# Kernel tuning notes

Measured on AMD Instinct MI355X. Metric: run time of the kernel, lower is better.

## Reference

```python
import jax, jax.numpy as jnp
import numpy as np

NEG_SLOPE = 0.2  # PyG GATConv default LeakyReLU slope


def gat_layer(x, src, dst, W, a_src, a_dst, bias, num_nodes, heads, out_ch, concat):
    # x: [N, in], W: [in, heads*out_ch], a_src/a_dst: [heads, out_ch]
    h = (x @ W).reshape(num_nodes, heads, out_ch)          # [N,H,C]
    alpha_s = jnp.sum(h * a_src, axis=-1)                  # [N,H]
    alpha_d = jnp.sum(h * a_dst, axis=-1)                  # [N,H]
    e = jax.nn.leaky_relu(alpha_s[src] + alpha_d[dst], NEG_SLOPE)  # [E,H]
    # softmax over incoming edges of each destination node
    e_max = jax.ops.segment_max(e, dst, num_segments=num_nodes)   # [N,H]
    e_exp = jnp.exp(e - e_max[dst])                        # [E,H]
    denom = jax.ops.segment_sum(e_exp, dst, num_segments=num_nodes)  # [N,H]
    alpha = e_exp / denom[dst]                             # [E,H]
    msg = h[src] * alpha[:, :, None]                       # [E,H,C]
    out = jax.ops.segment_sum(msg, dst, num_segments=num_nodes)     # [N,H,C]
    if concat:
        out = out.reshape(num_nodes, heads * out_ch)
    else:
        out = out.mean(axis=1)
    return out + bias


def setup_inputs() -> dict:
    key = jax.random.key(0)
    ks = jax.random.split(key, 12)
    N, E = 50000, 800000
    IN, HID, OUT, H = 128, 32, 64, 4
    x = jax.random.normal(ks[0], (N, IN), dtype=jnp.float32)
    edge_index = jax.random.randint(ks[1], (2, E), 0, N, dtype=jnp.int32)
    s = 1.0 / np.sqrt(IN)
    W1 = jax.random.normal(ks[2], (IN, H * HID), dtype=jnp.float32) * s
    a_src1 = jax.random.normal(ks[3], (H, HID), dtype=jnp.float32) * 0.1
    a_dst1 = jax.random.normal(ks[4], (H, HID), dtype=jnp.float32) * 0.1
    b1 = jnp.zeros((H * HID,), dtype=jnp.float32)
    s2 = 1.0 / np.sqrt(H * HID)
    W2 = jax.random.normal(ks[5], (H * HID, OUT), dtype=jnp.float32) * s2
    a_src2 = jax.random.normal(ks[6], (1, OUT), dtype=jnp.float32) * 0.1
    a_dst2 = jax.random.normal(ks[7], (1, OUT), dtype=jnp.float32) * 0.1
    b2 = jnp.zeros((OUT,), dtype=jnp.float32)
    return {"x": x, "edge_index": edge_index, "W1": W1, "a_src1": a_src1,
            "a_dst1": a_dst1, "b1": b1, "W2": W2, "a_src2": a_src2,
            "a_dst2": a_dst2, "b2": b2}


def reference(x, edge_index, W1, a_src1, a_dst1, b1, W2, a_src2, a_dst2, b2):
    N = x.shape[0]
    src, dst = edge_index[0], edge_index[1]
    h = gat_layer(x, src, dst, W1, a_src1, a_dst1, b1, N, heads=4, out_ch=32, concat=True)
    h = jax.nn.elu(h)
    # dropout is identity in eval / p=0.0
    out = gat_layer(h, src, dst, W2, a_src2, a_dst2, b2, N, heads=1, out_ch=64, concat=False)
    return out
```

## Files before the change

kernel.cpp:

```cpp
#include <hip/hip_runtime.h>

#define C1 128
#define C2 64
#define CAP 96
#define NBF 2048

typedef __attribute__((ext_vector_type(8))) _Float16 half8;
typedef __attribute__((ext_vector_type(2))) _Float16 half2v;
typedef __attribute__((ext_vector_type(2))) __fp16  fp16x2;
typedef __attribute__((ext_vector_type(4))) float floatx4;

__device__ __forceinline__ float lrelu(float v) { return v > 0.f ? v : 0.2f * v; }

__device__ __forceinline__ unsigned pk2h(float a, float b) {
    union { fp16x2 p; unsigned u; } c;
    c.p = __builtin_amdgcn_cvt_pkrtz(a, b);
    return c.u;
}

__global__ __launch_bounds__(256)
void gemm1_fill_kernel(const float* __restrict__ x, const float* __restrict__ W1,
                       const float* __restrict__ asrc, const float* __restrict__ adst,
                       unsigned* __restrict__ h1d,
                       float* __restrict__ as1, float* __restrict__ ad1,
                       const int* __restrict__ ei, int* __restrict__ cursor,
                       int* __restrict__ csrc, int nbTile, int N, int E) {
    if ((int)blockIdx.x >= nbTile) {
        const int b    = blockIdx.x - nbTile;
        const int part = b & 7;
        const int bIdx = b >> 3;
        const int bpp  = NBF >> 3;
        const int lo = (int)(((long)N * part) >> 3);
        const int hi = (int)(((long)N * (part + 1)) >> 3);

        const int E4 = ((E & 3) == 0) ? (E >> 2) : 0;
        const int4* d4 = (const int4*)(ei + E);
        const int4* s4 = (const int4*)ei;
        for (int q = bIdx * 256 + threadIdx.x; q < E4; q += bpp * 256) {
            int4 dv = d4[q];
            int4 sv = s4[q];
            int dd[4] = {dv.x, dv.y, dv.z, dv.w};
            int ss[4] = {sv.x, sv.y, sv.z, sv.w};
            int pos[4];
            bool act[4];
#pragma unroll
            for (int i = 0; i < 4; ++i) {
                act[i] = (dd[i] >= lo) & (dd[i] < hi) & ((unsigned)ss[i] < (unsigned)N);
                pos[i] = act[i] ? atomicAdd(&cursor[dd[i]], 1) : 0;
            }
#pragma unroll
            for (int i = 0; i < 4; ++i)
                if (act[i] && pos[i] < CAP) csrc[dd[i] * CAP + pos[i]] = ss[i];
        }
        for (int e = E4 * 4 + bIdx * 256 + threadIdx.x; e < E; e += bpp * 256) {
            int dd = ei[E + e];
            if (dd < lo || dd >= hi) continue;
            int ss = ei[e];
            if ((unsigned)ss >= (unsigned)N) continue;
            int pp = atomicAdd(&cursor[dd], 1);
            if (pp < CAP) csrc[dd * CAP + pp] = ss;
        }
        return;
    }

    __shared__ __align__(16) unsigned short Bs[128 * 136];
    for (int i = threadIdx.x; i < 128 * 64; i += 256) {
        int col = i & 127;
        int k = (i >> 7) * 2;
        *(unsigned*)&Bs[col * 136 + k] = pk2h(W1[k * 128 + col], W1[(k + 1) * 128 + col]);
    }
    __syncthreads();

    const int lane = threadIdx.x & 63, ww = threadIdx.x >> 6;
    const int quad = lane >> 4, l16 = lane & 15;
    const int nodeBase = blockIdx.x * 64 + ww * 16;
    int arow = nodeBase + l16;
    if (arow >= N) arow = N - 1;
    const float* xp = x + (size_t)arow * C1 + quad * 8;
    half8 afr[4];
#pragma unroll
    for (int kk = 0; kk < 4; ++kk) {
        float4 a0 = *(const float4*)(xp + kk * 32);
        float4 a1 = *(const float4*)(xp + kk * 32 + 4);
        union { half8 v; unsigned u[4]; } fr;
        fr.u[0] = pk2h(a0.x, a0.y);
        fr.u[1] = pk2h(a0.z, a0.w);
        fr.u[2] = pk2h(a1.x, a1.y);
        fr.u[3] = pk2h(a1.z, a1.w);
        afr[kk] = fr.v;
    }

#pragma unroll
    for (int h = 0; h < 4; ++h) {
        floatx4 accL = {0.f, 0.f, 0.f, 0.f};
        floatx4 accH = {0.f, 0.f, 0.f, 0.f};
        const int colL = h * 32 + l16;
        const int colH = colL + 16;
        const unsigned short* bL = &Bs[colL * 136 + quad * 8];
        const unsigned short* bH = &Bs[colH * 136 + quad * 8];
#pragma unroll
        for (int kk = 0; kk < 4; ++kk) {
            half8 bfrL = *(const half8*)(bL + kk * 32);
            half8 bfrH = *(const half8*)(bH + kk * 32);
            accL = __builtin_amdgcn_mfma_f32_16x16x32_f16(afr[kk], bfrL, accL, 0, 0, 0);
            accH = __builtin_amdgcn_mfma_f32_16x16x32_f16(afr[kk], bfrH, accH, 0, 0, 0);
        }
#pragma unroll
        for (int reg = 0; reg < 4; ++reg) {
            int node = nodeBase + quad * 4 + reg;
            if (node < N) h1d[(size_t)node * 64 + h * 16 + l16] = pk2h(accL[reg], accH[reg]);
        }
        float avL = asrc[colL], dvL = adst[colL];
        float avH = asrc[colH], dvH = adst[colH];
#pragma unroll
        for (int reg = 0; reg < 4; ++reg) {
            float ts = accL[reg] * avL + accH[reg] * avH;
            float td = accL[reg] * dvL + accH[reg] * dvH;
#pragma unroll
            for (int o = 1; o < 16; o <<= 1) {
                ts += __shfl_xor(ts, o, 64);
                td += __shfl_xor(td, o, 64);
            }
            if (l16 == 0) {
                int node = nodeBase + quad * 4 + reg;
                if (node < N) {
                    as1[node * 4 + h] = ts;
                    ad1[node * 4 + h] = td;
                }
            }
        }
    }
}

__global__ __launch_bounds__(256)
void msg1_csr_kernel(const int* __restrict__ cursor, const int* __restrict__ csrc,
                     const unsigned* __restrict__ h1u, const float* __restrict__ as1,
                     const float* __restrict__ ad1, const float* __restrict__ b1,
                     unsigned* __restrict__ out1, int N) {
    __shared__ float ws[4][64];
    const int wid = threadIdx.x >> 6;
    const int d = blockIdx.x * 4 + wid;
    if (d >= N) return;
    const int lane = threadIdx.x & 63;
    const int e16 = lane & 15;
    const int head = lane >> 4;
    int dg = cursor[d]; if (dg > CAP) dg = CAP;
    const int base = d * CAP;
    const float wadh = ad1[d * 4 + head];
    float accx = 0.f, accy = 0.f, sumw = 0.f;
    for (int jj = 0; jj < dg; jj += 16) {
        int idx = jj + e16;
        if (idx >= dg) idx = dg - 1;
        const int myS = csrc[base + idx];
        unsigned rv[16];
#pragma unroll
        for (int k = 0; k < 16; ++k) {
            int s = __builtin_amdgcn_readlane(myS, k);
            rv[k] = h1u[(unsigned)s * 64u + (unsigned)lane];
        }
        float w = 0.f;
        if (jj + e16 < dg)
            w = __expf(lrelu(as1[myS * 4 + head] + wadh));
        ws[wid][lane] = w;
#pragma unroll
        for (int j = 0; j < 4; ++j) {
            float4 wf = ((const float4*)&ws[wid][head * 16])[j];
            union { unsigned u; half2v p; } c0, c1, c2, c3;
            c0.u = rv[4 * j + 0]; c1.u = rv[4 * j + 1];
            c2.u = rv[4 * j + 2]; c3.u = rv[4 * j + 3];
            sumw += (wf.x + wf.y) + (wf.z + wf.w);
            accx += wf.x * (float)c0.p[0]; accy += wf.x * (float)c0.p[1];
            accx += wf.y * (float)c1.p[0]; accy += wf.y * (float)c1.p[1];
            accx += wf.z * (float)c2.p[0]; accy += wf.z * (float)c2.p[1];
            accx += wf.w * (float)c3.p[0]; accy += wf.w * (float)c3.p[1];
        }
    }
    float inv = (sumw > 0.f) ? 1.f / sumw : 0.f;
    float rx = accx * inv + b1[32 * head + e16];
    float ry = accy * inv + b1[32 * head + e16 + 16];
    rx = rx > 0.f ? rx : expm1f(rx);
    ry = ry > 0.f ? ry : expm1f(ry);
    out1[(size_t)d * 64 + lane] = pk2h(rx, ry);
}

__global__ __launch_bounds__(256)
void gemm2_mfma_kernel(const unsigned short* __restrict__ h2, const float* __restrict__ W2,
                       const float* __restrict__ asrc, const float* __restrict__ adst,
                       unsigned* __restrict__ g2d, float* __restrict__ as2,
                       float* __restrict__ ad2, int N) {
    __shared__ __align__(16) unsigned short Bs[64 * 136];
    for (int i = threadIdx.x; i < 64 * 64; i += 256) {
        int col = i & 63;
        int p = i >> 6;
        int k0 = 32 * (p >> 4) + (p & 15);
        *(unsigned*)&Bs[col * 136 + 2 * p] = pk2h(W2[k0 * 64 + col], W2[(k0 + 16) * 64 + col]);
    }
    __syncthreads();

    const int lane = threadIdx.x & 63, ww = threadIdx.x >> 6;
    const int quad = lane >> 4, l16 = lane & 15;
    const int nodeBase = blockIdx.x * 64 + ww * 16;
    int arow = nodeBase + l16;
    if (arow >= N) arow = N - 1;
    const unsigned short* xp = h2 + (size_t)arow * C1 + quad * 8;
    half8 afr[4];
#pragma unroll
    for (int kk = 0; kk < 4; ++kk)
        afr[kk] = *(const half8*)(xp + kk * 32);

    float sacc[4] = {0.f,0.f,0.f,0.f}, dacc[4] = {0.f,0.f,0.f,0.f};
#pragma unroll
    for (int ctp = 0; ctp < 2; ++ctp) {
        floatx4 accL = {0.f, 0.f, 0.f, 0.f};
        floatx4 accH = {0.f, 0.f, 0.f, 0.f};
        const int colL = ctp * 16 + l16;
        const int colH = colL + 32;
        const unsigned short* bL = &Bs[colL * 136 + quad * 8];
        const unsigned short* bH = &Bs[colH * 136 + quad * 8];
#pragma unroll
        for (int kk = 0; kk < 4; ++kk) {
            half8 bfrL = *(const half8*)(bL + kk * 32);
            half8 bfrH = *(const half8*)(bH + kk * 32);
            accL = __builtin_amdgcn_mfma_f32_16x16x32_f16(afr[kk], bfrL, accL, 0, 0, 0);
            accH = __builtin_amdgcn_mfma_f32_16x16x32_f16(afr[kk], bfrH, accH, 0, 0, 0);
        }
#pragma unroll
        for (int reg = 0; reg < 4; ++reg) {
            int node = nodeBase + quad * 4 + reg;
            if (node < N) g2d[(size_t)node * 32 + colL] = pk2h(accL[reg], accH[reg]);
        }
        float avL = asrc[colL], dvL = adst[colL];
        float avH = asrc[colH], dvH = adst[colH];
#pragma unroll
        for (int reg = 0; reg < 4; ++reg) {
            sacc[reg] += accL[reg] * avL + accH[reg] * avH;
            dacc[reg] += accL[reg] * dvL + accH[reg] * dvH;
        }
    }
#pragma unroll
    for (int reg = 0; reg < 4; ++reg) {
        float ts = sacc[reg], td = dacc[reg];
#pragma unroll
        for (int o = 1; o < 16; o <<= 1) {
            ts += __shfl_xor(ts, o, 64);
            td += __shfl_xor(td, o, 64);
        }
        if (l16 == 0) {
            int node = nodeBase + quad * 4 + reg;
            if (node < N) { as2[node] = ts; ad2[node] = td; }
        }
    }
}

__global__ __launch_bounds__(256)
void msg2_csr_kernel(const int* __restrict__ cursor, const int* __restrict__ csrc,
                     const unsigned* __restrict__ g2u, const float* __restrict__ as2,
                     const float* __restrict__ ad2, const float* __restrict__ b2,
                     float* __restrict__ yf, int N) {
    __shared__ float wsm[4][32];
    __shared__ int   ssm[4][32];
    const int wid = threadIdx.x >> 6;
    const int d = blockIdx.x * 4 + wid;
    if (d >= N) return;
    const int lane = threadIdx.x & 63;
    const int half = lane >> 5;
    const int l32 = lane & 31;
    int dg = cursor[d]; if (dg > CAP) dg = CAP;
    const int base = d * CAP;
    const float add = ad2[d];
    float accx = 0.f, accy = 0.f, sumw = 0.f;
    for (int jj = 0; jj < dg; jj += 32) {
        int idx = jj + l32;
        if (idx >= dg) idx = dg - 1;
        const int myS = csrc[base + idx];
        float w = 0.f;
        if (jj + l32 < dg) w = __expf(lrelu(as2[myS] + add));
        ssm[wid][l32] = myS;
        wsm[wid][l32] = w;
        int4 s0 = ((const int4*)&ssm[wid][half * 16])[0];
        int4 s1 = ((const int4*)&ssm[wid][half * 16])[1];
        int4 s2 = ((const int4*)&ssm[wid][half * 16])[2];
        int4 s3 = ((const int4*)&ssm[wid][half * 16])[3];
        int ss[16] = {s0.x, s0.y, s0.z, s0.w, s1.x, s1.y, s1.z, s1.w,
                      s2.x, s2.y, s2.z, s2.w, s3.x, s3.y, s3.z, s3.w};
        unsigned rv[16];
#pragma unroll
        for (int k = 0; k < 16; ++k)
            rv[k] = g2u[(unsigned)ss[k] * 32u + (unsigned)l32];
#pragma unroll
        for (int j = 0; j < 4; ++j) {
            float4 wf = ((const float4*)&wsm[wid][half * 16])[j];
            union { unsigned u; half2v p; } c0, c1, c2, c3;
            c0.u = rv[4 * j + 0]; c1.u = rv[4 * j + 1];
            c2.u = rv[4 * j + 2]; c3.u = rv[4 * j + 3];
            sumw += (wf.x + wf.y) + (wf.z + wf.w);
            accx += wf.x * (float)c0.p[0]; accy += wf.x * (float)c0.p[1];
            accx += wf.y * (float)c1.p[0]; accy += wf.y * (float)c1.p[1];
            accx += wf.z * (float)c2.p[0]; accy += wf.z * (float)c2.p[1];
            accx += wf.w * (float)c3.p[0]; accy += wf.w * (float)c3.p[1];
        }
    }
    accx += __shfl_xor(accx, 32, 64);
    accy += __shfl_xor(accy, 32, 64);
    sumw += __shfl_xor(sumw, 32, 64);
    if (half == 0) {
        float inv = (sumw > 0.f) ? 1.f / sumw : 0.f;
        yf[(size_t)d * 64 + l32]      = accx * inv + b2[l32];
        yf[(size_t)d * 64 + 32 + l32] = accy * inv + b2[l32 + 32];
    }
}

extern "C" void kernel_launch(void* const* d_in, const int* in_sizes, int n_in,
                              void* d_out, int out_size, void* d_ws, size_t ws_size,
                              hipStream_t stream) {
    const float* x    = (const float*)d_in[0];
    const int*   ei   = (const int*)d_in[1];
    const float* W1   = (const float*)d_in[2];
    const float* a_s1 = (const float*)d_in[3];
    const float* a_d1 = (const float*)d_in[4];
    const float* b1   = (const float*)d_in[5];
    const float* W2   = (const float*)d_in[6];
    const float* a_s2 = (const float*)d_in[7];
    const float* a_d2 = (const float*)d_in[8];
    const float* b2   = (const float*)d_in[9];

    const int N = in_sizes[0] / C1;
    const int E = in_sizes[1] / 2;

    auto align16 = [](size_t v) { return (v + 15) & ~(size_t)15; };
    const size_t RF   = 16;
    const size_t RCUR = align16((size_t)N * 4);
    const size_t RSRC = align16((size_t)N * CAP * 4);
    const size_t R1   = align16((size_t)N * C1 * 4);
    const size_t R2   = align16((size_t)N * 8 * 4);

    char* base = (char*)d_ws;
    int*  cursor = (int*)(base + RF);
    int*  csrc   = (int*)(base + RF + RCUR);
    char* R1p = base + RF + RCUR + RSRC;
    char* R2p = R1p + R1;
    char* R4p = R2p + R2;
    (void)ws_size;

    unsigned* h1 = (unsigned*)R1p;
    unsigned* g2 = (unsigned*)R1p;
    float* as1 = (float*)R2p;
    float* ad1 = as1 + (size_t)N * 4;
    float* as2 = (float*)R2p;
    float* ad2 = as2 + N;
    unsigned* out1 = (unsigned*)R4p;

    const int nbTile = (N + 63) / 64;
    const int nbWave4 = (N + 3) / 4;

    hipMemsetAsync(cursor, 0, (size_t)N * 4, stream);
    gemm1_fill_kernel<<<nbTile + NBF, 256, 0, stream>>>(x, W1, a_s1, a_d1, h1,
        as1, ad1, ei, cursor, csrc, nbTile, N, E);
    msg1_csr_kernel<<<nbWave4, 256, 0, stream>>>(cursor, csrc, (const unsigned*)h1,
        as1, ad1, b1, out1, N);
    gemm2_mfma_kernel<<<nbTile, 256, 0, stream>>>((const unsigned short*)out1, W2,
        a_s2, a_d2, g2, as2, ad2, N);
    msg2_csr_kernel<<<nbWave4, 256, 0, stream>>>(cursor, csrc, (const unsigned*)g2,
        as2, ad2, b2, (float*)d_out, N);
}
```

Measured before the change: 207.0 us.

## Interleave GEMM tiles with CSR-fill blocks and shrink msg2 gather batches

The fused gemm1/fill kernel used to put all GEMM tile blocks first and the CSR fill blocks after them. It now interleaves them in groups of eight, so compute-heavy tiles and atomic-heavy fill work run on the GPU at the same time instead of one phase after the other. Separately, msg2 now processes 16 neighbours per iteration instead of 32. Each half-wave takes alternate neighbours, using a transposed weight layout in shared memory. This aims to cut wasted gather and exp work for low-degree nodes, at the cost of more loop iterations and less load-level parallelism per iteration.

```diff
diff --git a/kernel.cpp b/kernel.cpp
--- a/kernel.cpp
+++ b/kernel.cpp
@@ -24,11 +24,17 @@
                        unsigned* __restrict__ h1d,
                        float* __restrict__ as1, float* __restrict__ ad1,
                        const int* __restrict__ ei, int* __restrict__ cursor,
-                       int* __restrict__ csrc, int nbTile, int N, int E) {
-    if ((int)blockIdx.x >= nbTile) {
-        const int b    = blockIdx.x - nbTile;
-        const int part = b & 7;
-        const int bIdx = b >> 3;
+                       int* __restrict__ csrc, int nbTile, int nbg, int kg, int ze,
+                       int N, int E) {
+    const int g   = blockIdx.x >> 3;
+    const int sub = blockIdx.x & 7;
+    int tile = -1, fg = -1;
+    if (g < ze && (g % kg) == 0) tile = (g / kg) * 8 + sub;
+    else fg = (g < ze) ? (g - g / kg - 1) : (g - nbg);
+
+    if (tile < 0) {
+        const int part = sub;
+        const int bIdx = fg;
         const int bpp  = NBF >> 3;
         const int lo = (int)(((long)N * part) >> 3);
         const int hi = (int)(((long)N * (part + 1)) >> 3);
@@ -62,6 +68,7 @@
         }
         return;
     }
+    if (tile >= nbTile) return;
 
     __shared__ __align__(16) unsigned short Bs[128 * 136];
     for (int i = threadIdx.x; i < 128 * 64; i += 256) {
@@ -73,7 +80,7 @@
 
     const int lane = threadIdx.x & 63, ww = threadIdx.x >> 6;
     const int quad = lane >> 4, l16 = lane & 15;
-    const int nodeBase = blockIdx.x * 64 + ww * 16;
+    const int nodeBase = tile * 64 + ww * 16;
     int arow = nodeBase + l16;
     if (arow >= N) arow = N - 1;
     const float* xp = x + (size_t)arow * C1 + quad * 8;
@@ -257,8 +264,8 @@
                      const unsigned* __restrict__ g2u, const float* __restrict__ as2,
                      const float* __restrict__ ad2, const float* __restrict__ b2,
                      float* __restrict__ yf, int N) {
-    __shared__ float wsm[4][32];
-    __shared__ int   ssm[4][32];
+    __shared__ float wsm[4][2][8];
+    __shared__ int   ssm[4][16];
     const int wid = threadIdx.x >> 6;
     const int d = blockIdx.x * 4 + wid;
     if (d >= N) return;
@@ -269,35 +276,29 @@
     const int base = d * CAP;
     const float add = ad2[d];
     float accx = 0.f, accy = 0.f, sumw = 0.f;
-    for (int jj = 0; jj < dg; jj += 32) {
-        int idx = jj + l32;
-        if (idx >= dg) idx = dg - 1;
-        const int myS = csrc[base + idx];
-        float w = 0.f;
-        if (jj + l32 < dg) w = __expf(lrelu(as2[myS] + add));
-        ssm[wid][l32] = myS;
-        wsm[wid][l32] = w;
-        int4 s0 = ((const int4*)&ssm[wid][half * 16])[0];
-        int4 s1 = ((const int4*)&ssm[wid][half * 16])[1];
-        int4 s2 = ((const int4*)&ssm[wid][half * 16])[2];
-        int4 s3 = ((const int4*)&ssm[wid][half * 16])[3];
-        int ss[16] = {s0.x, s0.y, s0.z, s0.w, s1.x, s1.y, s1.z, s1.w,
-                      s2.x, s2.y, s2.z, s2.w, s3.x, s3.y, s3.z, s3.w};
-        unsigned rv[16];
-#pragma unroll
-        for (int k = 0; k < 16; ++k)
-            rv[k] = g2u[(unsigned)ss[k] * 32u + (unsigned)l32];
-#pragma unroll
-        for (int j = 0; j < 4; ++j) {
-            float4 wf = ((const float4*)&wsm[wid][half * 16])[j];
-            union { unsigned u; half2v p; } c0, c1, c2, c3;
-            c0.u = rv[4 * j + 0]; c1.u = rv[4 * j + 1];
-            c2.u = rv[4 * j + 2]; c3.u = rv[4 * j + 3];
-            sumw += (wf.x + wf.y) + (wf.z + wf.w);
-            accx += wf.x * (float)c0.p[0]; accy += wf.x * (float)c0.p[1];
-            accx += wf.y * (float)c1.p[0]; accy += wf.y * (float)c1.p[1];
-            accx += wf.z * (float)c2.p[0]; accy += wf.z * (float)c2.p[1];
-            accx += wf.w * (float)c3.p[0]; accy += wf.w * (float)c3.p[1];
+    for (int jj = 0; jj < dg; jj += 16) {
+        if (l32 < 16) {
+            int idx = jj + l32;
+            if (idx >= dg) idx = dg - 1;
+            const int myS = csrc[base + idx];
+            float w = 0.f;
+            if (jj + l32 < dg) w = __expf(lrelu(as2[myS] + add));
+            ssm[wid][l32] = myS;
+            wsm[wid][l32 & 1][l32 >> 1] = w;
+        }
+        unsigned rv[8];
+#pragma unroll
+        for (int k = 0; k < 8; ++k)
+            rv[k] = g2u[(unsigned)ssm[wid][2 * k + half] * 32u + (unsigned)l32];
+        float4 wf0 = *(const float4*)&wsm[wid][half][0];
+        float4 wf1 = *(const float4*)&wsm[wid][half][4];
+        float wk[8] = {wf0.x, wf0.y, wf0.z, wf0.w, wf1.x, wf1.y, wf1.z, wf1.w};
+#pragma unroll
+        for (int k = 0; k < 8; ++k) {
+            union { unsigned u; half2v p; } c; c.u = rv[k];
+            sumw += wk[k];
+            accx += wk[k] * (float)c.p[0];
+            accy += wk[k] * (float)c.p[1];
         }
     }
     accx += __shfl_xor(accx, 32, 64);
@@ -353,9 +354,15 @@
     const int nbTile = (N + 63) / 64;
     const int nbWave4 = (N + 3) / 4;
 
+    const int nbg = (nbTile + 7) / 8;
+    const int nfg = NBF >> 3;
+    const int totalG = nbg + nfg;
+    const int kg = totalG / nbg;
+    const int ze = kg * nbg;
+
     hipMemsetAsync(cursor, 0, (size_t)N * 4, stream);
-    gemm1_fill_kernel<<<nbTile + NBF, 256, 0, stream>>>(x, W1, a_s1, a_d1, h1,
-        as1, ad1, ei, cursor, csrc, nbTile, N, E);
+    gemm1_fill_kernel<<<totalG * 8, 256, 0, stream>>>(x, W1, a_s1, a_d1, h1,
+        as1, ad1, ei, cursor, csrc, nbTile, nbg, kg, ze, N, E);
     msg1_csr_kernel<<<nbWave4, 256, 0, stream>>>(cursor, csrc, (const unsigned*)h1,
         as1, ad1, b1, out1, N);
     gemm2_mfma_kernel<<<nbTile, 256, 0, stream>>>((const unsigned short*)out1, W2,
```

Result: slower. 213.6 us (+3.2%).
